# Kernel tuning notes

Hardware: AMD Instinct MI355X
Metric: run time of the kernel (lower is better)

The kernel has to match this reference:

```python
import jax, jax.numpy as jnp
import numpy as np

D = 256
H = 4
HD = D // H


def rotate_half(x):
    xp = x.reshape(x.shape[:-1] + (-1, 2))
    x1, x2 = xp[..., 0], xp[..., 1]
    return jnp.stack((-x2, x1), axis=-1).reshape(x.shape)


def apply_rope(freqs, t):
    # freqs: [2, B, 1, N, HD]; t: [B, H, N, HD]
    return t * freqs[0] + rotate_half(t) * freqs[1]


def layernorm(x, g, b, eps=1e-5):
    m = jnp.mean(x, axis=-1, keepdims=True)
    v = jnp.var(x, axis=-1, keepdims=True)
    return (x - m) * jax.lax.rsqrt(v + eps) * g + b


def ffn(z, W1, b1, g, be, W2, b2):
    h = layernorm(z @ W1 + b1, g, be)
    h = jax.nn.gelu(h, approximate=False)
    return h @ W2 + b2


def heads_split(t):
    B, N, _ = t.shape
    return t.reshape(B, N, H, HD).transpose(0, 2, 1, 3)  # [B,H,N,HD]


def heads_merge(t):
    B, h, N, hd = t.shape
    return t.transpose(0, 2, 1, 3).reshape(B, N, h * hd)


def sdpa(q, k, v):
    s = q.shape[-1] ** (-0.5)
    sim = jnp.einsum('bhid,bhjd->bhij', q, k) * s
    attn = jax.nn.softmax(sim, axis=-1)
    return jnp.einsum('bhij,bhjd->bhid', attn, v)


def self_block(x, enc, Wqkv, bqkv, Wo, bo, W1, b1, g, be, W2, b2):
    B, N, _ = x.shape
    qkv = (x @ Wqkv + bqkv).reshape(B, N, H, HD, 3).transpose(0, 2, 1, 3, 4)
    q, k, v = qkv[..., 0], qkv[..., 1], qkv[..., 2]
    q = apply_rope(enc, q)
    k = apply_rope(enc, k)
    msg = heads_merge(sdpa(q, k, v)) @ Wo + bo
    return x + ffn(jnp.concatenate([x, msg], axis=-1), W1, b1, g, be, W2, b2)


def cross_block(x0, x1, Wqk, bqk, Wv, bv, Wo, bo, W1, b1, g, be, W2, b2):
    qk0 = heads_split(x0 @ Wqk + bqk)
    qk1 = heads_split(x1 @ Wqk + bqk)
    v0 = heads_split(x0 @ Wv + bv)
    v1 = heads_split(x1 @ Wv + bv)
    s = HD ** (-0.5)
    qk0 = qk0 * (s ** 0.5)
    qk1 = qk1 * (s ** 0.5)
    sim = jnp.einsum('bhid,bhjd->bhij', qk0, qk1)
    attn01 = jax.nn.softmax(sim, axis=-1)
    attn10 = jax.nn.softmax(sim.transpose(0, 1, 3, 2), axis=-1)
    m0 = jnp.einsum('bhij,bhjd->bhid', attn01, v1)
    m1 = jnp.einsum('bhij,bhjd->bhid', attn10, v0)
    m0 = heads_merge(m0) @ Wo + bo
    m1 = heads_merge(m1) @ Wo + bo
    x0 = x0 + ffn(jnp.concatenate([x0, m0], axis=-1), W1, b1, g, be, W2, b2)
    x1 = x1 + ffn(jnp.concatenate([x1, m1], axis=-1), W1, b1, g, be, W2, b2)
    return x0, x1


def setup_inputs() -> dict:
    key = jax.random.key(0)
    ks = jax.random.split(key, 24)
    B, N = 4, 2048
    desc0 = jax.random.normal(ks[0], (B, N, D), jnp.float32)
    desc1 = jax.random.normal(ks[1], (B, N, D), jnp.float32)
    encoding0 = jax.random.uniform(ks[2], (2, B, 1, N, HD), jnp.float32)
    encoding1 = jax.random.uniform(ks[3], (2, B, 1, N, HD), jnp.float32)

    def lin(k, fin, fout):
        k1, k2 = jax.random.split(k)
        W = jax.random.normal(k1, (fin, fout), jnp.float32) * (fin ** -0.5)
        b = jax.random.normal(k2, (fout,), jnp.float32) * 0.01
        return W, b

    Wqkv, bqkv = lin(ks[4], D, 3 * D)
    Wo_s, bo_s = lin(ks[5], D, D)
    W1_s, b1_s = lin(ks[6], 2 * D, 2 * D)
    g_s = jnp.ones((2 * D,), jnp.float32)
    be_s = jnp.zeros((2 * D,), jnp.float32)
    W2_s, b2_s = lin(ks[7], 2 * D, D)
    Wqk_c, bqk_c = lin(ks[8], D, D)
    Wv_c, bv_c = lin(ks[9], D, D)
    Wo_c, bo_c = lin(ks[10], D, D)
    W1_c, b1_c = lin(ks[11], 2 * D, 2 * D)
    g_c = jnp.ones((2 * D,), jnp.float32)
    be_c = jnp.zeros((2 * D,), jnp.float32)
    W2_c, b2_c = lin(ks[12], 2 * D, D)
    return dict(desc0=desc0, desc1=desc1, encoding0=encoding0, encoding1=encoding1,
                Wqkv=Wqkv, bqkv=bqkv, Wo_s=Wo_s, bo_s=bo_s,
                W1_s=W1_s, b1_s=b1_s, g_s=g_s, be_s=be_s, W2_s=W2_s, b2_s=b2_s,
                Wqk_c=Wqk_c, bqk_c=bqk_c, Wv_c=Wv_c, bv_c=bv_c, Wo_c=Wo_c, bo_c=bo_c,
                W1_c=W1_c, b1_c=b1_c, g_c=g_c, be_c=be_c, W2_c=W2_c, b2_c=b2_c)


def reference(desc0, desc1, encoding0, encoding1,
              Wqkv, bqkv, Wo_s, bo_s, W1_s, b1_s, g_s, be_s, W2_s, b2_s,
              Wqk_c, bqk_c, Wv_c, bv_c, Wo_c, bo_c, W1_c, b1_c, g_c, be_c, W2_c, b2_c):
    d0 = self_block(desc0, encoding0, Wqkv, bqkv, Wo_s, bo_s, W1_s, b1_s, g_s, be_s, W2_s, b2_s)
    d1 = self_block(desc1, encoding1, Wqkv, bqkv, Wo_s, bo_s, W1_s, b1_s, g_s, be_s, W2_s, b2_s)
    return cross_block(d0, d1, Wqk_c, bqk_c, Wv_c, bv_c, Wo_c, bo_c, W1_c, b1_c, g_c, be_c, W2_c, b2_c)
```

## Files before the change

### kernel.cpp

```cpp
#include <hip/hip_runtime.h>
#include <math.h>

#define BB 4
#define HH 4
#define NN 2048
#define DD 256
#define HDIM 64
#define NTOK 8192
#define NTOK2 16384

typedef __attribute__((ext_vector_type(8))) __bf16 bf16x8;
typedef __attribute__((ext_vector_type(8))) unsigned short ushort8;
typedef __attribute__((ext_vector_type(4))) float floatx4;
typedef __attribute__((ext_vector_type(4))) short short4v;

union U8 { ushort8 u; bf16x8 b; };
union U4 { unsigned int u[2]; unsigned long long l; short4v s; };

#define MFMA16(a, b, c) __builtin_amdgcn_mfma_f32_16x16x16bf16_1k(a, b, c, 0, 0, 0)

__device__ __forceinline__ unsigned short f2bf(float x) {
    unsigned int u = __float_as_uint(x);
    u += 0x7FFF + ((u >> 16) & 1);
    return (unsigned short)(u >> 16);
}
__device__ __forceinline__ float bf2f(unsigned short u) {
    return __uint_as_float(((unsigned int)u) << 16);
}
__device__ __forceinline__ unsigned int pkbf(float a, float b) {
    return ((__float_as_uint(a) + 0x8000u) >> 16) |
           ((__float_as_uint(b) + 0x8000u) & 0xFFFF0000u);
}

#define GLD(gp, lp) __builtin_amdgcn_global_load_lds( \
    (const __attribute__((address_space(1))) void*)(gp), \
    (__attribute__((address_space(3))) void*)(lp), 16, 0, 0)

struct WTab {
    const float* w[9];
    unsigned short* o[9];
    int K[9];
    int N[9];
    int t0[10];
};

__global__ __launch_bounds__(256) void wtrans(WTab tab)
{
    __shared__ float lds[32][33];
    const int t = threadIdx.x;
    int bid = blockIdx.x;
    int s = 0;
    while (bid >= tab.t0[s + 1]) s++;
    const int ti = bid - tab.t0[s];
    const int K = tab.K[s], N = tab.N[s];
    const int tx = ti % (N / 32), ty = ti / (N / 32);
    const int k0 = ty * 32, n0 = tx * 32;
    const float* W = tab.w[s];
    unsigned short* Wt = tab.o[s];

    {
        int r = t >> 3, c = (t & 7) * 4;
        float4 a = *(const float4*)&W[(size_t)(k0 + r) * N + n0 + c];
        lds[r][c] = a.x; lds[r][c+1] = a.y; lds[r][c+2] = a.z; lds[r][c+3] = a.w;
    }
    __syncthreads();
    {
        int n = t >> 3, kq = (t & 7) * 4;
        ushort4 p;
        p.x = f2bf(lds[kq+0][n]); p.y = f2bf(lds[kq+1][n]);
        p.z = f2bf(lds[kq+2][n]); p.w = f2bf(lds[kq+3][n]);
        *(ushort4*)&Wt[(size_t)(n0 + n) * K + k0 + kq] = p;
    }
}

__global__ __launch_bounds__(256) void gemm_mfma(
    const unsigned short* __restrict__ A, int lda,
    const unsigned short* __restrict__ Wt, int K,
    const float* __restrict__ bias, const float* __restrict__ bias2, int mode,
    float* outF, unsigned short* outH0, unsigned short* outH1,
    unsigned short* outH2,
    int ldc, const float* R0, const float* R1)
{
    __shared__ __align__(16) unsigned short As[128 * 32];
    __shared__ __align__(16) unsigned short Bs[128 * 32];
    const int t = threadIdx.x;
    const int w = t >> 6, lane = t & 63, quad = lane >> 4, l15 = lane & 15;
    const int m0 = blockIdx.y * 128, n0 = blockIdx.x * 128;
    const int wm = (w >> 1) * 64, wn = (w & 1) * 64;
    const int lr = lane >> 2, lc = (lane & 3) * 8;

    floatx4 acc[4][4];
    #pragma unroll
    for (int i = 0; i < 4; i++)
        #pragma unroll
        for (int j = 0; j < 4; j++) acc[i][j] = (floatx4){0.f, 0.f, 0.f, 0.f};

    for (int k0 = 0; k0 < K; k0 += 32) {
        GLD(A  + (size_t)(m0 + w * 32      + lr) * lda + k0 + lc, &As[(w * 32) * 32]);
        GLD(A  + (size_t)(m0 + w * 32 + 16 + lr) * lda + k0 + lc, &As[(w * 32 + 16) * 32]);
        GLD(Wt + (size_t)(n0 + w * 32      + lr) * K   + k0 + lc, &Bs[(w * 32) * 32]);
        GLD(Wt + (size_t)(n0 + w * 32 + 16 + lr) * K   + k0 + lc, &Bs[(w * 32 + 16) * 32]);
        __syncthreads();

        U8 af[4], bf[4];
        #pragma unroll
        for (int i = 0; i < 4; i++)
            af[i].u = *(const ushort8*)&As[(wm + i * 16 + l15) * 32 + quad * 8];
        #pragma unroll
        for (int j = 0; j < 4; j++)
            bf[j].u = *(const ushort8*)&Bs[(wn + j * 16 + l15) * 32 + quad * 8];
        #pragma unroll
        for (int i = 0; i < 4; i++)
            #pragma unroll
            for (int j = 0; j < 4; j++)
                acc[i][j] = __builtin_amdgcn_mfma_f32_16x16x32_bf16(af[i].b, bf[j].b, acc[i][j], 0, 0, 0);
        __syncthreads();
    }

    #pragma unroll
    for (int i = 0; i < 4; i++) {
        #pragma unroll
        for (int j = 0; j < 4; j++) {
            int col = n0 + wn + j * 16 + l15;
            float bv = (mode == 2 && col >= 256) ? bias2[col & 255] : bias[col];
            #pragma unroll
            for (int r = 0; r < 4; r++) {
                int grow = m0 + wm + i * 16 + quad * 4 + r;
                float v = acc[i][j][r] + bv;
                if (mode == 1) {
                    outH0[(size_t)grow * ldc + col] = f2bf(v);
                } else if (mode == 2) {
                    int cc = col & 255;
                    int h = cc >> 6, d = cc & 63;
                    int ds = grow >> 13, b = (grow >> 11) & 3, n = grow & 2047;
                    int bh = ds * 16 + b * 4 + h;
                    unsigned short* dst = (col < 256) ? outH0 : outH1;
                    dst[((size_t)bh * NN + n) * HDIM + d] = f2bf(v);
                } else if (mode == 3) {
                    int sel = col % 3, cc = col / 3;
                    int h = cc >> 6, d = cc & 63;
                    int ds = grow >> 13, b = (grow >> 11) & 3, n = grow & 2047;
                    int bh = ds * 16 + b * 4 + h;
                    unsigned short* dst = (sel == 0) ? outH0 : ((sel == 1) ? outH1 : outH2);
                    dst[((size_t)bh * NN + n) * HDIM + d] = f2bf(v);
                } else {
                    const float* R = (grow < NTOK) ? R0 : R1;
                    float vv = v + R[(size_t)(grow & 8191) * 256 + col];
                    outF[(size_t)grow * 256 + col] = vv;
                    if (outH0) outH0[(size_t)grow * 256 + col] = f2bf(vv);
                    if (outH1) outH1[(size_t)grow * 512 + col] = f2bf(vv);
                }
            }
        }
    }
}

__global__ __launch_bounds__(256) void rope_k(unsigned short* __restrict__ qb,
                                              unsigned short* __restrict__ kb,
                                              const float* __restrict__ enc0,
                                              const float* __restrict__ enc1)
{
    int i = blockIdx.x * 256 + threadIdx.x;
    int dp = (i & 31) * 2;
    int n  = (i >> 5) & (NN - 1);
    int h  = (i >> 16) & 3;
    int b  = (i >> 18) & 3;
    int ds = (i >> 20) & 1;
    int bf = (i >> 21) & 1;
    unsigned short* tq = (bf ? kb : qb) +
        (((size_t)(ds * 16 + b * 4 + h)) * NN + n) * HDIM + dp;
    const float* e0 = (ds ? enc1 : enc0) + ((size_t)b * NN + n) * HDIM + dp;
    const float* e1 = e0 + (size_t)BB * NN * HDIM;
    float x0 = bf2f(tq[0]), x1 = bf2f(tq[1]);
    float y0 = x0 * e0[0] - x1 * e1[0];
    float y1 = x1 * e0[1] + x0 * e1[1];
    tq[0] = f2bf(y0); tq[1] = f2bf(y1);
}

__global__ __launch_bounds__(256) void flash_attn(
    const unsigned short* __restrict__ Q, const unsigned short* __restrict__ K,
    const unsigned short* __restrict__ V, unsigned short* __restrict__ O,
    int kvx, float qscale)
{
    __shared__ __align__(16) unsigned short Ks[64 * 72];
    __shared__ __align__(16) unsigned short Vt[64 * 72];

    const int t    = threadIdx.x;
    const int w    = t >> 6;
    const int lane = t & 63;
    const int quad = lane >> 4;
    const int l15  = lane & 15;
    const int bh   = blockIdx.y;
    const int kbh  = bh ^ kvx;
    const int q0   = blockIdx.x * 64;

    const unsigned short* Qb = Q + (size_t)bh  * NN * HDIM;
    const unsigned short* Kb = K + (size_t)kbh * NN * HDIM;
    const unsigned short* Vb = V + (size_t)kbh * NN * HDIM;

    const int qrow = q0 + w * 16 + l15;
    bf16x8 qf0, qf1;
    {
        U8 r0, r1, x0, x1;
        r0.u = *(const ushort8*)&Qb[(size_t)qrow * HDIM + quad * 8];
        r1.u = *(const ushort8*)&Qb[(size_t)qrow * HDIM + 32 + quad * 8];
        #pragma unroll
        for (int j = 0; j < 8; j++) {
            x0.u[j] = f2bf(bf2f(r0.u[j]) * qscale);
            x1.u[j] = f2bf(bf2f(r1.u[j]) * qscale);
        }
        qf0 = x0.b; qf1 = x1.b;
    }

    floatx4 o[4];
    #pragma unroll
    for (int c = 0; c < 4; c++) o[c] = (floatx4){0.f, 0.f, 0.f, 0.f};
    float m = -1e30f, l = 0.f;

    for (int j0 = 0; j0 < NN; j0 += 64) {
        #pragma unroll
        for (int f = t; f < 512; f += 256) {
            int r = f >> 3, ch = (f & 7) * 8;
            *(ushort8*)&Ks[r * 72 + ch] =
                *(const ushort8*)&Kb[(size_t)(j0 + r) * HDIM + ch];
        }
        #pragma unroll
        for (int f = t; f < 512; f += 256) {
            int kp = f & 31, c4 = (f >> 5) * 4;
            ushort4 v0 = *(const ushort4*)&Vb[(size_t)(j0 + 2 * kp) * HDIM + c4];
            ushort4 v1 = *(const ushort4*)&Vb[(size_t)(j0 + 2 * kp + 1) * HDIM + c4];
            *(unsigned int*)&Vt[(c4 + 0) * 72 + 2 * kp] = (unsigned int)v0.x | ((unsigned int)v1.x << 16);
            *(unsigned int*)&Vt[(c4 + 1) * 72 + 2 * kp] = (unsigned int)v0.y | ((unsigned int)v1.y << 16);
            *(unsigned int*)&Vt[(c4 + 2) * 72 + 2 * kp] = (unsigned int)v0.z | ((unsigned int)v1.z << 16);
            *(unsigned int*)&Vt[(c4 + 3) * 72 + 2 * kp] = (unsigned int)v0.w | ((unsigned int)v1.w << 16);
        }
        __syncthreads();

        floatx4 s[4];
        #pragma unroll
        for (int t4 = 0; t4 < 4; t4++) {
            U8 k0, k1;
            k0.u = *(const ushort8*)&Ks[(t4 * 16 + l15) * 72 + quad * 8];
            k1.u = *(const ushort8*)&Ks[(t4 * 16 + l15) * 72 + 32 + quad * 8];
            floatx4 z = (floatx4){0.f, 0.f, 0.f, 0.f};
            z = __builtin_amdgcn_mfma_f32_16x16x32_bf16(k0.b, qf0, z, 0, 0, 0);
            z = __builtin_amdgcn_mfma_f32_16x16x32_bf16(k1.b, qf1, z, 0, 0, 0);
            s[t4] = z;
        }

        float mx = s[0][0];
        #pragma unroll
        for (int t4 = 0; t4 < 4; t4++)
            #pragma unroll
            for (int r = 0; r < 4; r++) mx = fmaxf(mx, s[t4][r]);
        mx = fmaxf(mx, __shfl_xor(mx, 16, 64));
        mx = fmaxf(mx, __shfl_xor(mx, 32, 64));
        float mn = fmaxf(m, mx);
        float al = exp2f(m - mn);
        m = mn;
        float rs = 0.f;
        #pragma unroll
        for (int t4 = 0; t4 < 4; t4++)
            #pragma unroll
            for (int r = 0; r < 4; r++) {
                float p = exp2f(s[t4][r] - mn);
                s[t4][r] = p;
                rs += p;
            }
        rs += __shfl_xor(rs, 16, 64);
        rs += __shfl_xor(rs, 32, 64);
        l = l * al + rs;
        #pragma unroll
        for (int c = 0; c < 4; c++)
            #pragma unroll
            for (int r = 0; r < 4; r++) o[c][r] *= al;

        short4v pf[4];
        #pragma unroll
        for (int t4 = 0; t4 < 4; t4++) {
            U4 pk;
            pk.u[0] = pkbf(s[t4][0], s[t4][1]);
            pk.u[1] = pkbf(s[t4][2], s[t4][3]);
            pf[t4] = pk.s;
        }

        #pragma unroll
        for (int c = 0; c < 4; c++) {
            #pragma unroll
            for (int t4 = 0; t4 < 4; t4++) {
                U4 vf;
                vf.l = *(const unsigned long long*)
                    &Vt[(c * 16 + l15) * 72 + t4 * 16 + quad * 4];
                o[c] = MFMA16(vf.s, pf[t4], o[c]);
            }
        }
        __syncthreads();
    }

    const int ds = bh >> 4, b = (bh >> 2) & 3, h = bh & 3;
    const int q = q0 + w * 16 + l15;
    const size_t row = (size_t)ds * NTOK + b * NN + q;
    float inv = 1.f / l;
    #pragma unroll
    for (int c = 0; c < 4; c++) {
        ushort4 pk;
        pk.x = f2bf(o[c][0] * inv);
        pk.y = f2bf(o[c][1] * inv);
        pk.z = f2bf(o[c][2] * inv);
        pk.w = f2bf(o[c][3] * inv);
        *(ushort4*)&O[row * DD + h * HDIM + c * 16 + quad * 4] = pk;
    }
}

__global__ __launch_bounds__(256) void ln_gelu(
    unsigned short* __restrict__ hb, const float* __restrict__ g,
    const float* __restrict__ be)
{
    __shared__ float r1[4], r2[4];
    const int t = threadIdx.x;
    const size_t row = blockIdx.x;
    unsigned short* ip = hb + row * 512;
    float x0 = bf2f(ip[t]), x1 = bf2f(ip[t + 256]);
    float s = x0 + x1, ss = x0 * x0 + x1 * x1;
    #pragma unroll
    for (int o = 32; o > 0; o >>= 1) { s += __shfl_down(s, o); ss += __shfl_down(ss, o); }
    if ((t & 63) == 0) { r1[t >> 6] = s; r2[t >> 6] = ss; }
    __syncthreads();
    float S  = r1[0] + r1[1] + r1[2] + r1[3];
    float SS = r2[0] + r2[1] + r2[2] + r2[3];
    float mean = S * (1.f / 512.f);
    float var  = SS * (1.f / 512.f) - mean * mean;
    float inv  = rsqrtf(var + 1e-5f);
    float y0 = (x0 - mean) * inv * g[t]       + be[t];
    float y1 = (x1 - mean) * inv * g[t + 256] + be[t + 256];
    ip[t]       = f2bf(0.5f * y0 * (1.f + erff(y0 * 0.70710678f)));
    ip[t + 256] = f2bf(0.5f * y1 * (1.f + erff(y1 * 0.70710678f)));
}

__global__ __launch_bounds__(256) void copy_to_cat(
    const float* __restrict__ s0, const float* __restrict__ s1,
    unsigned short* __restrict__ cat)
{
    int i = blockIdx.x * 256 + threadIdx.x;
    int row = i >> 6, c4 = (i & 63) * 4;
    const float* s = (row < NTOK) ? s0 : s1;
    float4 a = *(const float4*)&s[(size_t)(row & 8191) * 256 + c4];
    ushort4 p = { f2bf(a.x), f2bf(a.y), f2bf(a.z), f2bf(a.w) };
    *(ushort4*)&cat[(size_t)row * 512 + c4] = p;
}

extern "C" void kernel_launch(void* const* d_in, const int* in_sizes, int n_in,
                              void* d_out, int out_size, void* d_ws, size_t ws_size,
                              hipStream_t stream)
{
    const float* desc0 = (const float*)d_in[0];
    const float* desc1 = (const float*)d_in[1];
    const float* enc0  = (const float*)d_in[2];
    const float* enc1  = (const float*)d_in[3];
    const float* Wqkv  = (const float*)d_in[4];  const float* bqkv  = (const float*)d_in[5];
    const float* Wo_s  = (const float*)d_in[6];  const float* bo_s  = (const float*)d_in[7];
    const float* W1_s  = (const float*)d_in[8];  const float* b1_s  = (const float*)d_in[9];
    const float* g_s   = (const float*)d_in[10]; const float* be_s  = (const float*)d_in[11];
    const float* W2_s  = (const float*)d_in[12]; const float* b2_s  = (const float*)d_in[13];
    const float* Wqk_c = (const float*)d_in[14]; const float* bqk_c = (const float*)d_in[15];
    const float* Wv_c  = (const float*)d_in[16]; const float* bv_c  = (const float*)d_in[17];
    const float* Wo_c  = (const float*)d_in[18]; const float* bo_c  = (const float*)d_in[19];
    const float* W1_c  = (const float*)d_in[20]; const float* b1_c  = (const float*)d_in[21];
    const float* g_c   = (const float*)d_in[22]; const float* be_c  = (const float*)d_in[23];
    const float* W2_c  = (const float*)d_in[24]; const float* b2_c  = (const float*)d_in[25];

    char* ws = (char*)d_ws;
    unsigned short* wt  = (unsigned short*)ws;
    unsigned short* qb  = (unsigned short*)(ws + 2490368);
    unsigned short* kb  = (unsigned short*)(ws + 10878976);
    unsigned short* msg = (unsigned short*)(ws + 19267584);
    unsigned short* vb  = (unsigned short*)(ws + 27656192);
    unsigned short* cat = (unsigned short*)(ws + 36044800);
    unsigned short* hb  = (unsigned short*)(ws + 52822016);
    unsigned short* dbf = (unsigned short*)(ws + 86376448);

    unsigned short* t_qkv = wt;
    unsigned short* t_wos = wt + 196608;
    unsigned short* t_w1s = wt + 262144;
    unsigned short* t_w2s = wt + 524288;
    unsigned short* t_wqk = wt + 655360;
    unsigned short* t_wv  = wt + 720896;
    unsigned short* t_woc = wt + 786432;
    unsigned short* t_w1c = wt + 851968;
    unsigned short* t_w2c = wt + 1114112;

    float* outF = (float*)d_out;

    dim3 blk(256);

    WTab tab;
    tab.w[0] = Wqkv;  tab.o[0] = t_qkv; tab.K[0] = 256; tab.N[0] = 768;
    tab.w[1] = Wo_s;  tab.o[1] = t_wos; tab.K[1] = 256; tab.N[1] = 256;
    tab.w[2] = W1_s;  tab.o[2] = t_w1s; tab.K[2] = 512; tab.N[2] = 512;
    tab.w[3] = W2_s;  tab.o[3] = t_w2s; tab.K[3] = 512; tab.N[3] = 256;
    tab.w[4] = Wqk_c; tab.o[4] = t_wqk; tab.K[4] = 256; tab.N[4] = 256;
    tab.w[5] = Wv_c;  tab.o[5] = t_wv;  tab.K[5] = 256; tab.N[5] = 256;
    tab.w[6] = Wo_c;  tab.o[6] = t_woc; tab.K[6] = 256; tab.N[6] = 256;
    tab.w[7] = W1_c;  tab.o[7] = t_w1c; tab.K[7] = 512; tab.N[7] = 512;
    tab.w[8] = W2_c;  tab.o[8] = t_w2c; tab.K[8] = 512; tab.N[8] = 256;
    int acc_t = 0;
    for (int s = 0; s < 9; s++) {
        tab.t0[s] = acc_t;
        acc_t += (tab.K[s] / 32) * (tab.N[s] / 32);
    }
    tab.t0[9] = acc_t;
    hipLaunchKernelGGL(wtrans, dim3(acc_t), blk, 0, stream, tab);

    auto gemm = [&](const unsigned short* A, int lda, const unsigned short* Wtp,
                    int K, const float* bias, const float* bias2, int Nc, int mode,
                    float* oF, unsigned short* oh0, unsigned short* oh1,
                    unsigned short* oh2, int ldc, const float* r0, const float* r1) {
        dim3 g(Nc / 128, NTOK2 / 128);
        hipLaunchKernelGGL(gemm_mfma, g, blk, 0, stream,
                           A, lda, Wtp, K, bias, bias2, mode,
                           oF, oh0, oh1, oh2, ldc, r0, r1);
    };

    const float QS = 0.125f * 1.44269504088896f;

    hipLaunchKernelGGL(copy_to_cat, dim3(4096), blk, 0, stream, desc0, desc1, cat);
    gemm(cat, 512, t_qkv, 256, bqkv, nullptr, 768, 3,
         nullptr, qb, kb, vb, 0, nullptr, nullptr);
    hipLaunchKernelGGL(rope_k, dim3(16384), blk, 0, stream, qb, kb, enc0, enc1);
    hipLaunchKernelGGL(flash_attn, dim3(NN / 64, 32), blk, 0, stream,
                       qb, kb, vb, msg, 0, QS);
    gemm(msg, 256, t_wos, 256, bo_s, nullptr, 256, 1,
         nullptr, cat + 256, nullptr, nullptr, 512, nullptr, nullptr);
    gemm(cat, 512, t_w1s, 512, b1_s, nullptr, 512, 1,
         nullptr, hb, nullptr, nullptr, 512, nullptr, nullptr);
    hipLaunchKernelGGL(ln_gelu, dim3(NTOK2), blk, 0, stream, hb, g_s, be_s);
    gemm(hb, 512, t_w2s, 512, b2_s, nullptr, 256, 4,
         outF, dbf, cat, nullptr, 256, desc0, desc1);

    gemm(dbf, 256, t_wqk, 256, bqk_c, bv_c, 512, 2,
         nullptr, qb, vb, nullptr, 0, nullptr, nullptr);
    hipLaunchKernelGGL(flash_attn, dim3(NN / 64, 32), blk, 0, stream,
                       qb, qb, vb, msg, 16, QS);
    gemm(msg, 256, t_woc, 256, bo_c, nullptr, 256, 1,
         nullptr, cat + 256, nullptr, nullptr, 512, nullptr, nullptr);
    gemm(cat, 512, t_w1c, 512, b1_c, nullptr, 512, 1,
         nullptr, hb, nullptr, nullptr, 512, nullptr, nullptr);
    hipLaunchKernelGGL(ln_gelu, dim3(NTOK2), blk, 0, stream, hb, g_c, be_c);
    gemm(hb, 512, t_w2c, 512, b2_c, nullptr, 256, 4,
         outF, nullptr, nullptr, nullptr, 256, outF, outF + (size_t)NTOK * 256);
}
```

Measured before the change: 557.2 us.

## Prefetch tiles into registers and write V pre-transposed from projection GEMMs

The GEMM replaces direct global-to-LDS loads with register prefetch of the next K tile while the current one is computed, and pads LDS rows to 40 elements to avoid bank conflicts. The projection epilogues now write V in a [bh][d][n] transposed layout, so the flash attention kernel can copy V tiles straight into LDS with vector loads instead of transposing them in-kernel. Attention also prefetches the next K/V tile into registers. In exchange it uses more registers and makes the V stores scattered with a stride of NN in the epilogue.

```diff
diff --git a/kernel.cpp b/kernel.cpp
--- a/kernel.cpp
+++ b/kernel.cpp
@@ -31,10 +31,6 @@
     return ((__float_as_uint(a) + 0x8000u) >> 16) |
            ((__float_as_uint(b) + 0x8000u) & 0xFFFF0000u);
 }
-
-#define GLD(gp, lp) __builtin_amdgcn_global_load_lds( \
-    (const __attribute__((address_space(1))) void*)(gp), \
-    (__attribute__((address_space(3))) void*)(lp), 16, 0, 0)
 
 struct WTab {
     const float* w[9];
@@ -81,13 +77,21 @@
     unsigned short* outH2,
     int ldc, const float* R0, const float* R1)
 {
-    __shared__ __align__(16) unsigned short As[128 * 32];
-    __shared__ __align__(16) unsigned short Bs[128 * 32];
+    __shared__ __align__(16) unsigned short As[128 * 40];
+    __shared__ __align__(16) unsigned short Bs[128 * 40];
     const int t = threadIdx.x;
     const int w = t >> 6, lane = t & 63, quad = lane >> 4, l15 = lane & 15;
     const int m0 = blockIdx.y * 128, n0 = blockIdx.x * 128;
     const int wm = (w >> 1) * 64, wn = (w & 1) * 64;
-    const int lr = lane >> 2, lc = (lane & 3) * 8;
+    const int sr = t >> 1, sc = (t & 1) * 16;
+
+    const unsigned short* Ap = A  + (size_t)(m0 + sr) * lda + sc;
+    const unsigned short* Bp = Wt + (size_t)(n0 + sr) * K   + sc;
+
+    ushort8 pa0 = *(const ushort8*)(Ap);
+    ushort8 pa1 = *(const ushort8*)(Ap + 8);
+    ushort8 pb0 = *(const ushort8*)(Bp);
+    ushort8 pb1 = *(const ushort8*)(Bp + 8);
 
     floatx4 acc[4][4];
     #pragma unroll
@@ -95,20 +99,27 @@
         #pragma unroll
         for (int j = 0; j < 4; j++) acc[i][j] = (floatx4){0.f, 0.f, 0.f, 0.f};
 
-    for (int k0 = 0; k0 < K; k0 += 32) {
-        GLD(A  + (size_t)(m0 + w * 32      + lr) * lda + k0 + lc, &As[(w * 32) * 32]);
-        GLD(A  + (size_t)(m0 + w * 32 + 16 + lr) * lda + k0 + lc, &As[(w * 32 + 16) * 32]);
-        GLD(Wt + (size_t)(n0 + w * 32      + lr) * K   + k0 + lc, &Bs[(w * 32) * 32]);
-        GLD(Wt + (size_t)(n0 + w * 32 + 16 + lr) * K   + k0 + lc, &Bs[(w * 32 + 16) * 32]);
+    const int nk = K >> 5;
+    for (int kk = 0; kk < nk; kk++) {
+        *(ushort8*)&As[sr * 40 + sc]     = pa0;
+        *(ushort8*)&As[sr * 40 + sc + 8] = pa1;
+        *(ushort8*)&Bs[sr * 40 + sc]     = pb0;
+        *(ushort8*)&Bs[sr * 40 + sc + 8] = pb1;
         __syncthreads();
-
+        if (kk + 1 < nk) {
+            int ko = (kk + 1) * 32;
+            pa0 = *(const ushort8*)(Ap + ko);
+            pa1 = *(const ushort8*)(Ap + ko + 8);
+            pb0 = *(const ushort8*)(Bp + ko);
+            pb1 = *(const ushort8*)(Bp + ko + 8);
+        }
         U8 af[4], bf[4];
         #pragma unroll
         for (int i = 0; i < 4; i++)
-            af[i].u = *(const ushort8*)&As[(wm + i * 16 + l15) * 32 + quad * 8];
+            af[i].u = *(const ushort8*)&As[(wm + i * 16 + l15) * 40 + quad * 8];
         #pragma unroll
         for (int j = 0; j < 4; j++)
-            bf[j].u = *(const ushort8*)&Bs[(wn + j * 16 + l15) * 32 + quad * 8];
+            bf[j].u = *(const ushort8*)&Bs[(wn + j * 16 + l15) * 40 + quad * 8];
         #pragma unroll
         for (int i = 0; i < 4; i++)
             #pragma unroll
@@ -134,15 +145,21 @@
                     int h = cc >> 6, d = cc & 63;
                     int ds = grow >> 13, b = (grow >> 11) & 3, n = grow & 2047;
                     int bh = ds * 16 + b * 4 + h;
-                    unsigned short* dst = (col < 256) ? outH0 : outH1;
-                    dst[((size_t)bh * NN + n) * HDIM + d] = f2bf(v);
+                    if (col < 256)
+                        outH0[((size_t)bh * NN + n) * HDIM + d] = f2bf(v);
+                    else
+                        outH1[((size_t)bh * HDIM + d) * NN + n] = f2bf(v);
                 } else if (mode == 3) {
                     int sel = col % 3, cc = col / 3;
                     int h = cc >> 6, d = cc & 63;
                     int ds = grow >> 13, b = (grow >> 11) & 3, n = grow & 2047;
                     int bh = ds * 16 + b * 4 + h;
-                    unsigned short* dst = (sel == 0) ? outH0 : ((sel == 1) ? outH1 : outH2);
-                    dst[((size_t)bh * NN + n) * HDIM + d] = f2bf(v);
+                    if (sel == 0)
+                        outH0[((size_t)bh * NN + n) * HDIM + d] = f2bf(v);
+                    else if (sel == 1)
+                        outH1[((size_t)bh * NN + n) * HDIM + d] = f2bf(v);
+                    else
+                        outH2[((size_t)bh * HDIM + d) * NN + n] = f2bf(v);
                 } else {
                     const float* R = (grow < NTOK) ? R0 : R1;
                     float vv = v + R[(size_t)(grow & 8191) * 256 + col];
@@ -194,9 +211,11 @@
     const int kbh  = bh ^ kvx;
     const int q0   = blockIdx.x * 64;
 
-    const unsigned short* Qb = Q + (size_t)bh  * NN * HDIM;
-    const unsigned short* Kb = K + (size_t)kbh * NN * HDIM;
-    const unsigned short* Vb = V + (size_t)kbh * NN * HDIM;
+    const unsigned short* Qb  = Q + (size_t)bh  * NN * HDIM;
+    const unsigned short* Kb  = K + (size_t)kbh * NN * HDIM;
+    const unsigned short* VTb = V + (size_t)kbh * NN * HDIM;
+
+    const int srf = t >> 3, scf = (t & 7) * 8;
 
     const int qrow = q0 + w * 16 + l15;
     bf16x8 qf0, qf1;
@@ -217,24 +236,24 @@
     for (int c = 0; c < 4; c++) o[c] = (floatx4){0.f, 0.f, 0.f, 0.f};
     float m = -1e30f, l = 0.f;
 
+    ushort8 ka0 = *(const ushort8*)&Kb[(size_t)srf * HDIM + scf];
+    ushort8 ka1 = *(const ushort8*)&Kb[(size_t)(srf + 32) * HDIM + scf];
+    ushort8 va0 = *(const ushort8*)&VTb[(size_t)srf * NN + scf];
+    ushort8 va1 = *(const ushort8*)&VTb[(size_t)(srf + 32) * NN + scf];
+
     for (int j0 = 0; j0 < NN; j0 += 64) {
-        #pragma unroll
-        for (int f = t; f < 512; f += 256) {
-            int r = f >> 3, ch = (f & 7) * 8;
-            *(ushort8*)&Ks[r * 72 + ch] =
-                *(const ushort8*)&Kb[(size_t)(j0 + r) * HDIM + ch];
-        }
-        #pragma unroll
-        for (int f = t; f < 512; f += 256) {
-            int kp = f & 31, c4 = (f >> 5) * 4;
-            ushort4 v0 = *(const ushort4*)&Vb[(size_t)(j0 + 2 * kp) * HDIM + c4];
-            ushort4 v1 = *(const ushort4*)&Vb[(size_t)(j0 + 2 * kp + 1) * HDIM + c4];
-            *(unsigned int*)&Vt[(c4 + 0) * 72 + 2 * kp] = (unsigned int)v0.x | ((unsigned int)v1.x << 16);
-            *(unsigned int*)&Vt[(c4 + 1) * 72 + 2 * kp] = (unsigned int)v0.y | ((unsigned int)v1.y << 16);
-            *(unsigned int*)&Vt[(c4 + 2) * 72 + 2 * kp] = (unsigned int)v0.z | ((unsigned int)v1.z << 16);
-            *(unsigned int*)&Vt[(c4 + 3) * 72 + 2 * kp] = (unsigned int)v0.w | ((unsigned int)v1.w << 16);
-        }
+        *(ushort8*)&Ks[srf * 72 + scf]        = ka0;
+        *(ushort8*)&Ks[(srf + 32) * 72 + scf] = ka1;
+        *(ushort8*)&Vt[srf * 72 + scf]        = va0;
+        *(ushort8*)&Vt[(srf + 32) * 72 + scf] = va1;
         __syncthreads();
+        if (j0 + 64 < NN) {
+            int jn = j0 + 64;
+            ka0 = *(const ushort8*)&Kb[(size_t)(jn + srf) * HDIM + scf];
+            ka1 = *(const ushort8*)&Kb[(size_t)(jn + srf + 32) * HDIM + scf];
+            va0 = *(const ushort8*)&VTb[(size_t)srf * NN + jn + scf];
+            va1 = *(const ushort8*)&VTb[(size_t)(srf + 32) * NN + jn + scf];
+        }
 
         floatx4 s[4];
         #pragma unroll
```

Result: faster. 533.3 us (-4.3%).
